# Optimization experiments

Hardware: AMD Instinct MI355X
Metric: run time of the kernel (lower is better)

## Reference

```python
import jax, jax.numpy as jnp
import numpy as np

N_AGENTS = 16
OBS_DIM = 256
ACT_DIM = 32
B, T = 16, 64
ADAPTIVE = max(10, N_AGENTS)  # 16 Monte-Carlo counterfactual samples
H1, H2 = 128, 64


def setup_inputs() -> dict:
    key = jax.random.key(0)
    ks = jax.random.split(key, 10)
    in_dim = OBS_DIM + ACT_DIM
    inp = {
        "obs": jax.random.normal(ks[0], (B, T, N_AGENTS, OBS_DIM), dtype=jnp.float32),
        "actions": jax.random.uniform(ks[1], (B, T, N_AGENTS, ACT_DIM), dtype=jnp.float32),
        "cf_actions": jax.random.uniform(ks[2], (N_AGENTS, ADAPTIVE, B, T, ACT_DIM), dtype=jnp.float32),
        "W1": jax.random.normal(ks[3], (in_dim, H1), dtype=jnp.float32) / np.sqrt(in_dim),
        "b1": jnp.zeros((H1,), dtype=jnp.float32),
        "W2": jax.random.normal(ks[4], (H1, H2), dtype=jnp.float32) / np.sqrt(H1),
        "b2": jnp.zeros((H2,), dtype=jnp.float32),
        "W3": jax.random.normal(ks[5], (H2, ACT_DIM), dtype=jnp.float32) / np.sqrt(H2),
        "b3": jnp.zeros((ACT_DIM,), dtype=jnp.float32),
    }
    return inp


def _mlp(x, W1, b1, W2, b2, W3, b3):
    h = jax.nn.relu(x @ W1 + b1)
    h = jax.nn.relu(h @ W2 + b2)
    return h @ W3 + b3


def reference(obs, actions, cf_actions, W1, b1, W2, b2, W3, b3):
    # obs: [B,T,N,D], actions: [B,T,N,A], cf_actions: [N,S,B,T,A]
    obs_n = jnp.moveaxis(obs, 2, 0)      # [N,B,T,D]
    act_n = jnp.moveaxis(actions, 2, 0)  # [N,B,T,A]

    # p(with k): MLP([obs_k, action_k]) for all agents at once  -> [N,B,T,A]
    p_with = _mlp(jnp.concatenate([obs_n, act_n], axis=-1), W1, b1, W2, b2, W3, b3)
    # p(zero action)
    p_zero = _mlp(jnp.concatenate([obs_n, jnp.zeros_like(act_n)], axis=-1),
                  W1, b1, W2, b2, W3, b3)
    # Monte-Carlo counterfactuals: [N,S,B,T,A]
    S = cf_actions.shape[1]
    obs_rep = jnp.broadcast_to(obs_n[:, None], (obs_n.shape[0], S) + obs_n.shape[1:])
    p_cf = _mlp(jnp.concatenate([obs_rep, cf_actions], axis=-1), W1, b1, W2, b2, W3, b3)

    p_without = (p_zero + p_cf.sum(axis=1)) / (S + 1)  # [N,B,T,A]

    # F.kl_div(log_softmax(p_with), softmax(p_without), reduction='none')
    log_p = jax.nn.log_softmax(p_with, axis=-1)
    q = jax.nn.softmax(p_without, axis=-1)
    log_q = jax.nn.log_softmax(p_without, axis=-1)
    kl = q * (log_q - log_p)  # [N,B,T,A]

    # stack over agents on last dim then mean over action dim -> [B,T,N]
    influences = jnp.moveaxis(kl.mean(axis=-1), 0, -1)
    return influences
```

## Files before the change

### kernel.cpp

```cpp
#include <hip/hip_runtime.h>

#define NAG   16
#define OBSD  256
#define ACTD  32
#define SCF   16
#define H1D   128
#define H2D   64
#define BT    1024
#define NTOK  16384
#define CFS   32768
#define NEVAL 18

typedef float f4 __attribute__((ext_vector_type(4)));

#define OBS_OFF  0
#define BS_OFF   8192
#define ACT_OFF  0
#define W1S_OFF  1152
#define W2S_OFF  5248
#define HS_OFF   13440
#define H2S_OFF  17664
#define LDS_FLOATS 19840

__global__ __launch_bounds__(256, 2) void k_fused(
    const float* __restrict__ obs, const float* __restrict__ actions,
    const float* __restrict__ cf, const float* __restrict__ W1,
    const float* __restrict__ b1, const float* __restrict__ W2,
    const float* __restrict__ b2v, const float* __restrict__ W3,
    const float* __restrict__ b3v, float* __restrict__ out)
{
    __shared__ float lds[LDS_FLOATS];

    const int tid = threadIdx.x;
    const int g0  = blockIdx.x * 32;

    const int rb1 = tid >> 5, cb1 = tid & 31;
    const int rb2 = tid >> 4, cb2 = tid & 15;
    const int r3  = tid >> 3, cb3 = tid & 7;

    {
        const float* src = obs + g0 * OBSD;
        #pragma unroll
        for (int j = 0; j < 8; ++j) {
            int idx = tid + j * 256;
            *(f4*)(lds + OBS_OFF + idx * 4) = *(const f4*)(src + idx * 4);
        }
    }

    float acc[4][4] = {};
    for (int kt = 0; kt < OBSD; kt += 32) {
        __syncthreads();
        const float* wsrc = W1 + kt * H1D;
        #pragma unroll
        for (int u = 0; u < 4; ++u)
            *(f4*)(lds + BS_OFF + u * 1024 + tid * 4) =
                *(const f4*)(wsrc + u * 1024 + tid * 4);
        __syncthreads();
        #pragma unroll
        for (int k0 = 0; k0 < 32; k0 += 4) {
            f4 a[4], b[4];
            #pragma unroll
            for (int i = 0; i < 4; ++i)
                a[i] = *(const f4*)(lds + OBS_OFF + (rb1 * 4 + i) * OBSD + kt + k0);
            #pragma unroll
            for (int kk = 0; kk < 4; ++kk)
                b[kk] = *(const f4*)(lds + BS_OFF + (k0 + kk) * H1D + cb1 * 4);
            #pragma unroll
            for (int i = 0; i < 4; ++i)
                #pragma unroll
                for (int kk = 0; kk < 4; ++kk)
                    #pragma unroll
                    for (int j = 0; j < 4; ++j)
                        acc[i][j] = fmaf(a[i][kk], b[kk][j], acc[i][j]);
        }
    }
    f4 hobs[4];
    {
        f4 bias = *(const f4*)(b1 + cb1 * 4);
        #pragma unroll
        for (int i = 0; i < 4; ++i)
            #pragma unroll
            for (int j = 0; j < 4; ++j)
                hobs[i][j] = acc[i][j] + bias[j];
    }
    __syncthreads();

    #pragma unroll
    for (int u = 0; u < 4; ++u)
        *(f4*)(lds + W1S_OFF + u * 1024 + tid * 4) =
            *(const f4*)(W1 + OBSD * H1D + u * 1024 + tid * 4);
    #pragma unroll
    for (int u = 0; u < 8; ++u)
        *(f4*)(lds + W2S_OFF + u * 1024 + tid * 4) =
            *(const f4*)(W2 + u * 1024 + tid * 4);

    f4 bias2 = *(const f4*)(b2v + cb2 * 4);
    f4 bias3 = *(const f4*)(b3v + cb3 * 4);

    const int atok = tid >> 3;
    const int aa   = (tid & 7) * 4;
    const int g_at = g0 + atok;
    const int n_at = g_at & (NAG - 1);
    const int bt_at = g_at >> 4;

    f4 pw = {0.f, 0.f, 0.f, 0.f};
    f4 pq = {0.f, 0.f, 0.f, 0.f};

    __syncthreads();

    for (int e = 0; e < NEVAL; ++e) {
        if (e != 1) {
            const float* src;
            if (e == 0) src = actions + g_at * ACTD + aa;
            else        src = cf + (n_at * SCF + (e - 2)) * CFS + bt_at * ACTD + aa;
            *(f4*)(lds + ACT_OFF + atok * 36 + aa) = *(const f4*)src;
        }
        __syncthreads();

        f4 hv[4];
        if (e != 1) {
            float a1c[4][4] = {};
            #pragma unroll
            for (int k0 = 0; k0 < ACTD; k0 += 4) {
                f4 a[4], b[4];
                #pragma unroll
                for (int i = 0; i < 4; ++i)
                    a[i] = *(const f4*)(lds + ACT_OFF + (rb1 * 4 + i) * 36 + k0);
                #pragma unroll
                for (int kk = 0; kk < 4; ++kk)
                    b[kk] = *(const f4*)(lds + W1S_OFF + (k0 + kk) * H1D + cb1 * 4);
                #pragma unroll
                for (int i = 0; i < 4; ++i)
                    #pragma unroll
                    for (int kk = 0; kk < 4; ++kk)
                        #pragma unroll
                        for (int j = 0; j < 4; ++j)
                            a1c[i][j] = fmaf(a[i][kk], b[kk][j], a1c[i][j]);
            }
            #pragma unroll
            for (int i = 0; i < 4; ++i)
                #pragma unroll
                for (int j = 0; j < 4; ++j)
                    hv[i][j] = fmaxf(hobs[i][j] + a1c[i][j], 0.f);
        } else {
            #pragma unroll
            for (int i = 0; i < 4; ++i)
                #pragma unroll
                for (int j = 0; j < 4; ++j)
                    hv[i][j] = fmaxf(hobs[i][j], 0.f);
        }
        #pragma unroll
        for (int i = 0; i < 4; ++i)
            *(f4*)(lds + HS_OFF + (rb1 * 4 + i) * 132 + cb1 * 4) = hv[i];
        __syncthreads();

        {
            float acc2[2][4] = {};
            const int t0 = rb2 * 2, t1 = rb2 * 2 + 1;
            #pragma unroll 8
            for (int k0 = 0; k0 < H1D; k0 += 4) {
                f4 a0 = *(const f4*)(lds + HS_OFF + t0 * 132 + k0);
                f4 a1 = *(const f4*)(lds + HS_OFF + t1 * 132 + k0);
                f4 b[4];
                #pragma unroll
                for (int kk = 0; kk < 4; ++kk)
                    b[kk] = *(const f4*)(lds + W2S_OFF + (k0 + kk) * H2D + cb2 * 4);
                #pragma unroll
                for (int kk = 0; kk < 4; ++kk)
                    #pragma unroll
                    for (int j = 0; j < 4; ++j) {
                        acc2[0][j] = fmaf(a0[kk], b[kk][j], acc2[0][j]);
                        acc2[1][j] = fmaf(a1[kk], b[kk][j], acc2[1][j]);
                    }
            }
            f4 v0, v1;
            #pragma unroll
            for (int j = 0; j < 4; ++j) {
                v0[j] = fmaxf(acc2[0][j] + bias2[j], 0.f);
                v1[j] = fmaxf(acc2[1][j] + bias2[j], 0.f);
            }
            *(f4*)(lds + H2S_OFF + t0 * 68 + cb2 * 4) = v0;
            *(f4*)(lds + H2S_OFF + t1 * 68 + cb2 * 4) = v1;
        }
        __syncthreads();

        {
            f4 a3 = {0.f, 0.f, 0.f, 0.f};
            #pragma unroll 8
            for (int k0 = 0; k0 < H2D; k0 += 4) {
                f4 a = *(const f4*)(lds + H2S_OFF + r3 * 68 + k0);
                #pragma unroll
                for (int kk = 0; kk < 4; ++kk) {
                    f4 b = *(const f4*)(W3 + (k0 + kk) * ACTD + cb3 * 4);
                    #pragma unroll
                    for (int j = 0; j < 4; ++j)
                        a3[j] = fmaf(a[kk], b[j], a3[j]);
                }
            }
            #pragma unroll
            for (int j = 0; j < 4; ++j) a3[j] += bias3[j];
            if (e == 0) pw = a3;
            else {
                #pragma unroll
                for (int j = 0; j < 4; ++j) pq[j] += a3[j];
            }
        }
        __syncthreads();
    }

    const float inv17 = 1.0f / 17.0f;
    f4 qv;
    #pragma unroll
    for (int j = 0; j < 4; ++j) qv[j] = pq[j] * inv17;

    float mw = fmaxf(fmaxf(pw[0], pw[1]), fmaxf(pw[2], pw[3]));
    float mq = fmaxf(fmaxf(qv[0], qv[1]), fmaxf(qv[2], qv[3]));
    #pragma unroll
    for (int m = 1; m < 8; m <<= 1) {
        mw = fmaxf(mw, __shfl_xor(mw, m));
        mq = fmaxf(mq, __shfl_xor(mq, m));
    }
    float sw = 0.f, sq = 0.f;
    #pragma unroll
    for (int j = 0; j < 4; ++j) {
        sw += expf(pw[j] - mw);
        sq += expf(qv[j] - mq);
    }
    #pragma unroll
    for (int m = 1; m < 8; m <<= 1) {
        sw += __shfl_xor(sw, m);
        sq += __shfl_xor(sq, m);
    }
    const float lsw = logf(sw), lsq = logf(sq);
    float kl = 0.f;
    #pragma unroll
    for (int j = 0; j < 4; ++j) {
        float lq = qv[j] - mq - lsq;
        float lp = pw[j] - mw - lsw;
        kl += expf(lq) * (lq - lp);
    }
    #pragma unroll
    for (int m = 1; m < 8; m <<= 1) kl += __shfl_xor(kl, m);

    if (cb3 == 0) out[g0 + r3] = kl * (1.0f / 32.0f);
}

extern "C" void kernel_launch(void* const* d_in, const int* in_sizes, int n_in,
                              void* d_out, int out_size, void* d_ws, size_t ws_size,
                              hipStream_t stream)
{
    const float* obs     = (const float*)d_in[0];
    const float* actions = (const float*)d_in[1];
    const float* cf      = (const float*)d_in[2];
    const float* W1      = (const float*)d_in[3];
    const float* b1      = (const float*)d_in[4];
    const float* W2      = (const float*)d_in[5];
    const float* b2      = (const float*)d_in[6];
    const float* W3      = (const float*)d_in[7];
    const float* b3      = (const float*)d_in[8];
    float* outp = (float*)d_out;

    k_fused<<<NTOK / 32, 256, 0, stream>>>(obs, actions, cf, W1, b1, W2,
                                           b2, W3, b3, outp);
}
```

Before: 265.1 us.

## Read actions directly from global, split-K layer 2 with XOR-swizzled LDS

Drops the LDS staging of action vectors and the barrier that went with it, so each thread loads its four action rows straight from global memory during the layer-1 action GEMM. Layer 2 becomes a split-K scheme: two halves of the block each compute a 4x4 register tile over half of K, then combine partial sums through LDS. The padded LDS rows are replaced by XOR swizzles to avoid bank conflicts, which shrinks LDS use. The cost is redundant global loads of actions across the 32 threads sharing rows, plus an extra barrier and a read-modify-write for the split-K reduction.

```diff
diff --git a/kernel.cpp b/kernel.cpp
--- a/kernel.cpp
+++ b/kernel.cpp
@@ -8,19 +8,20 @@
 #define H2D   64
 #define BT    1024
 #define NTOK  16384
-#define CFS   32768
 #define NEVAL 18
 
 typedef float f4 __attribute__((ext_vector_type(4)));
 
 #define OBS_OFF  0
 #define BS_OFF   8192
-#define ACT_OFF  0
-#define W1S_OFF  1152
-#define W2S_OFF  5248
-#define HS_OFF   13440
-#define H2S_OFF  17664
-#define LDS_FLOATS 19840
+#define W1S_OFF  0
+#define W2S_OFF  4096
+#define HS_OFF   12288
+#define H2S_OFF  16384
+#define LDS_FLOATS 18432
+
+#define X1(r) (((r) & 7) << 2)
+#define X2(r) (((r) & 7) << 3)
 
 __global__ __launch_bounds__(256, 2) void k_fused(
     const float* __restrict__ obs, const float* __restrict__ actions,
@@ -35,8 +36,10 @@
     const int g0  = blockIdx.x * 32;
 
     const int rb1 = tid >> 5, cb1 = tid & 31;
-    const int rb2 = tid >> 4, cb2 = tid & 15;
-    const int r3  = tid >> 3, cb3 = tid & 7;
+    const int kh = tid >> 7;
+    const int rg = (tid >> 4) & 7;
+    const int cg = tid & 15;
+    const int r3 = tid >> 3, cb3 = tid & 7;
 
     {
         const float* src = obs + g0 * OBSD;
@@ -94,14 +97,12 @@
         *(f4*)(lds + W2S_OFF + u * 1024 + tid * 4) =
             *(const f4*)(W2 + u * 1024 + tid * 4);
 
-    f4 bias2 = *(const f4*)(b2v + cb2 * 4);
+    f4 bias2 = *(const f4*)(b2v + cg * 4);
     f4 bias3 = *(const f4*)(b3v + cb3 * 4);
 
-    const int atok = tid >> 3;
-    const int aa   = (tid & 7) * 4;
-    const int g_at = g0 + atok;
-    const int n_at = g_at & (NAG - 1);
-    const int bt_at = g_at >> 4;
+    const int row0 = rb1 * 4;
+    const int n0   = row0 & 15;
+    const int btt  = (g0 >> 4) + (row0 >> 4);
 
     f4 pw = {0.f, 0.f, 0.f, 0.f};
     f4 pq = {0.f, 0.f, 0.f, 0.f};
@@ -109,23 +110,23 @@
     __syncthreads();
 
     for (int e = 0; e < NEVAL; ++e) {
-        if (e != 1) {
-            const float* src;
-            if (e == 0) src = actions + g_at * ACTD + aa;
-            else        src = cf + (n_at * SCF + (e - 2)) * CFS + bt_at * ACTD + aa;
-            *(f4*)(lds + ACT_OFF + atok * 36 + aa) = *(const f4*)src;
-        }
-        __syncthreads();
-
         f4 hv[4];
         if (e != 1) {
+            const float* asrc;
+            int astride;
+            if (e == 0) { asrc = actions + (g0 + row0) * ACTD; astride = ACTD; }
+            else {
+                asrc = cf + n0 * (SCF * BT * ACTD) + (e - 2) * (BT * ACTD)
+                          + btt * ACTD;
+                astride = SCF * BT * ACTD;
+            }
             float a1c[4][4] = {};
             #pragma unroll
             for (int k0 = 0; k0 < ACTD; k0 += 4) {
                 f4 a[4], b[4];
                 #pragma unroll
                 for (int i = 0; i < 4; ++i)
-                    a[i] = *(const f4*)(lds + ACT_OFF + (rb1 * 4 + i) * 36 + k0);
+                    a[i] = *(const f4*)(asrc + i * astride + k0);
                 #pragma unroll
                 for (int kk = 0; kk < 4; ++kk)
                     b[kk] = *(const f4*)(lds + W1S_OFF + (k0 + kk) * H1D + cb1 * 4);
@@ -150,37 +151,56 @@
                     hv[i][j] = fmaxf(hobs[i][j], 0.f);
         }
         #pragma unroll
-        for (int i = 0; i < 4; ++i)
-            *(f4*)(lds + HS_OFF + (rb1 * 4 + i) * 132 + cb1 * 4) = hv[i];
-        __syncthreads();
-
+        for (int i = 0; i < 4; ++i) {
+            int r = rb1 * 4 + i;
+            *(f4*)(lds + HS_OFF + r * H1D + ((cb1 * 4) ^ X1(r))) = hv[i];
+        }
+        __syncthreads();
+
+        float acc2[4][4] = {};
         {
-            float acc2[2][4] = {};
-            const int t0 = rb2 * 2, t1 = rb2 * 2 + 1;
+            const int kb = kh * 64;
             #pragma unroll 8
-            for (int k0 = 0; k0 < H1D; k0 += 4) {
-                f4 a0 = *(const f4*)(lds + HS_OFF + t0 * 132 + k0);
-                f4 a1 = *(const f4*)(lds + HS_OFF + t1 * 132 + k0);
-                f4 b[4];
+            for (int k0 = 0; k0 < 64; k0 += 4) {
+                f4 a[4], b[4];
+                #pragma unroll
+                for (int i = 0; i < 4; ++i) {
+                    int r = rg * 4 + i;
+                    a[i] = *(const f4*)(lds + HS_OFF + r * H1D + ((kb + k0) ^ X1(r)));
+                }
                 #pragma unroll
                 for (int kk = 0; kk < 4; ++kk)
-                    b[kk] = *(const f4*)(lds + W2S_OFF + (k0 + kk) * H2D + cb2 * 4);
-                #pragma unroll
-                for (int kk = 0; kk < 4; ++kk)
-                    #pragma unroll
-                    for (int j = 0; j < 4; ++j) {
-                        acc2[0][j] = fmaf(a0[kk], b[kk][j], acc2[0][j]);
-                        acc2[1][j] = fmaf(a1[kk], b[kk][j], acc2[1][j]);
-                    }
-            }
-            f4 v0, v1;
-            #pragma unroll
-            for (int j = 0; j < 4; ++j) {
-                v0[j] = fmaxf(acc2[0][j] + bias2[j], 0.f);
-                v1[j] = fmaxf(acc2[1][j] + bias2[j], 0.f);
-            }
-            *(f4*)(lds + H2S_OFF + t0 * 68 + cb2 * 4) = v0;
-            *(f4*)(lds + H2S_OFF + t1 * 68 + cb2 * 4) = v1;
+                    b[kk] = *(const f4*)(lds + W2S_OFF + (kb + k0 + kk) * H2D + cg * 4);
+                #pragma unroll
+                for (int i = 0; i < 4; ++i)
+                    #pragma unroll
+                    for (int kk = 0; kk < 4; ++kk)
+                        #pragma unroll
+                        for (int j = 0; j < 4; ++j)
+                            acc2[i][j] = fmaf(a[i][kk], b[kk][j], acc2[i][j]);
+            }
+        }
+        if (kh) {
+            #pragma unroll
+            for (int i = 0; i < 4; ++i) {
+                int r = rg * 4 + i;
+                f4 v = {acc2[i][0], acc2[i][1], acc2[i][2], acc2[i][3]};
+                *(f4*)(lds + H2S_OFF + r * H2D + ((cg * 4) ^ X2(r))) = v;
+            }
+        }
+        __syncthreads();
+        if (!kh) {
+            #pragma unroll
+            for (int i = 0; i < 4; ++i) {
+                int r = rg * 4 + i;
+                float* p = lds + H2S_OFF + r * H2D + ((cg * 4) ^ X2(r));
+                f4 part = *(const f4*)p;
+                f4 v;
+                #pragma unroll
+                for (int j = 0; j < 4; ++j)
+                    v[j] = fmaxf(acc2[i][j] + part[j] + bias2[j], 0.f);
+                *(f4*)p = v;
+            }
         }
         __syncthreads();
 
@@ -188,7 +208,7 @@
             f4 a3 = {0.f, 0.f, 0.f, 0.f};
             #pragma unroll 8
             for (int k0 = 0; k0 < H2D; k0 += 4) {
-                f4 a = *(const f4*)(lds + H2S_OFF + r3 * 68 + k0);
+                f4 a = *(const f4*)(lds + H2S_OFF + r3 * H2D + (k0 ^ X2(r3)));
                 #pragma unroll
                 for (int kk = 0; kk < 4; ++kk) {
                     f4 b = *(const f4*)(W3 + (k0 + kk) * ACTD + cb3 * 4);
```

After: 264.1 us. No clear change (-0.3%).
